# Optimization experiments

Hardware: AMD Instinct MI355X
Metric: run time of the kernel (lower is better)

Reference implementation:

```python
import jax, jax.numpy as jnp
import numpy as np

SIZE = 128      # reconstruction grid (size x size)
ANGLES = 128    # number of projection angles after interpolation
B, C, H, W = 2, 8, 128, 128  # batch, channels, detector rows (z-slices), detector cols
N_VIEWS = 8


def setup_inputs() -> dict:
    key = jax.random.key(0)
    keys = jax.random.split(key, N_VIEWS)
    return {f"f{i}": jax.random.normal(keys[i], (B, C, H, W), dtype=jnp.float32)
            for i in range(N_VIEWS)}


def _fbp(projections, size, n_angles):
    # projections: (B, C, H, V, W) -- V stacked views, W detector columns
    b, c, h, v, w = projections.shape
    # Interpolation step: resize V views -> n_angles angles (linear, half-pixel,
    # matching F.interpolate default semantics)
    sino = jax.image.resize(projections, (b, c, h, n_angles, w), method="linear")
    # Ram-Lak ramp filter along the detector-column axis
    ramp = jnp.abs(jnp.fft.fftfreq(w)).astype(jnp.float32)
    filt = jnp.real(jnp.fft.ifft(jnp.fft.fft(sino, axis=-1) * ramp, axis=-1)).astype(sino.dtype)
    # Back-projection (parallel beam, per z-slice H)
    thetas = jnp.arange(n_angles, dtype=jnp.float32) * (jnp.pi / n_angles)
    xs = jnp.arange(size, dtype=jnp.float32) - (size - 1) / 2.0
    X, Y = jnp.meshgrid(xs, xs, indexing="xy")  # (S, S)
    center = (w - 1) / 2.0

    sino_per_angle = jnp.moveaxis(filt, 3, 0)  # (A, B, C, H, W)

    def body(acc, inputs):
        theta, sino_a = inputs                       # sino_a: (B, C, H, W)
        t = X * jnp.cos(theta) + Y * jnp.sin(theta) + center  # (S, S)
        t = jnp.clip(t, 0.0, w - 1.0)
        t0 = jnp.floor(t).astype(jnp.int32)
        t1 = jnp.minimum(t0 + 1, w - 1)
        w1 = (t - t0).astype(sino_a.dtype)
        v0 = sino_a[..., t0]                         # (B, C, H, S, S) gather
        v1 = sino_a[..., t1]
        acc = acc + v0 * (1.0 - w1) + v1 * w1
        return acc, None

    acc0 = jnp.zeros((b, c, h, size, size), dtype=sino.dtype)
    vol, _ = jax.lax.scan(body, acc0, (thetas, sino_per_angle))
    return vol * (jnp.pi / (2.0 * n_angles))


def reference(f0, f1, f2, f3, f4, f5, f6, f7):
    # torch.cat([f.unsqueeze(3) for f in features], dim=3) == stack on new axis 3
    projections = jnp.stack([f0, f1, f2, f3, f4, f5, f6, f7], axis=3)  # (B,C,H,V,W)
    return _fbp(projections, SIZE, ANGLES)
```

## Files before the change

### kernel.cpp

```cpp
#include <hip/hip_runtime.h>
#include <math.h>

#define W 128
#define NANG 128
#define SZ 128
#define NV 8
#define NROWS 2048
#define K_DIM 1024
#define NPIX 16384
#define OUT_SCALE 0.012271846303085130f

typedef _Float16 f16x8 __attribute__((ext_vector_type(8)));
typedef _Float16 f16x4 __attribute__((ext_vector_type(4)));
typedef float    f32x4 __attribute__((ext_vector_type(4)));

#define PF_OFF 36864
#define WV_OFF (36864 + (size_t)NROWS * K_DIM * 2)

struct Ptrs8 { const float* p[8]; };

__device__ __forceinline__ void glds16(const void* g, void* l) {
    __builtin_amdgcn_global_load_lds(
        (const __attribute__((address_space(1))) void*)g,
        (__attribute__((address_space(3))) void*)l, 16, 0, 0);
}

#define FS_A 136
#define PREP_FG_BLOCKS 256

union PrepLds {
    struct {
        _Float16 sA[64 * FS_A];
        _Float16 sB[128 * FS_A];
        float    kl[W];
    } fg;
    struct {
        float  wrow[8 * K_DIM];
        float2 cst[NANG];
    } wv;
};

__global__ __launch_bounds__(256)
void k_prep(Ptrs8 in, _Float16* __restrict__ pf, _Float16* __restrict__ wv) {
    __shared__ PrepLds u;
    const int tid = threadIdx.x;

    if (blockIdx.x < PREP_FG_BLOCKS) {
        const int blk  = blockIdx.x;
        const int lane = tid & 63, wave = tid >> 6;
        const int fr = lane & 15, fg = lane >> 4;

        if (tid < W) {
            const int d = tid;
            const float w0 = 6.283185307179586f / (float)W * (float)d;
            float s = 0.f;
            for (int f = 1; f < 64; ++f)
                s = fmaf((float)f, __cosf(w0 * (float)f), s);
            s = 2.f * s + 64.f * ((d & 1) ? -1.f : 1.f);
            u.fg.kl[d] = s * (1.f / (float)(W * W));
        }
        {
            const int i   = tid >> 5;
            const int pos = (tid & 31) * 4;
#pragma unroll
            for (int v = 0; v < NV; ++v) {
                float4 x = *(const float4*)(in.p[v] + (size_t)(blk * 8 + i) * W + pos);
                f16x4 h = { (_Float16)x.x, (_Float16)x.y, (_Float16)x.z, (_Float16)x.w };
                *(f16x4*)&u.fg.sA[(i * 8 + v) * FS_A + pos] = h;
            }
        }
        __syncthreads();
        for (int e = tid; e < W * W; e += 256) {
            const int t = e >> 7, s = e & 127;
            u.fg.sB[t * FS_A + s] = (_Float16)u.fg.kl[(t - s) & (W - 1)];
        }
        __syncthreads();

        f32x4 acc[8] = {};
#pragma unroll
        for (int kb = 0; kb < W; kb += 32) {
            f16x8 af = *(const f16x8*)&u.fg.sA[(wave * 16 + fr) * FS_A + kb + fg * 8];
#pragma unroll
            for (int nt = 0; nt < 8; ++nt) {
                f16x8 bf = *(const f16x8*)&u.fg.sB[(nt * 16 + fr) * FS_A + kb + fg * 8];
                acc[nt] = __builtin_amdgcn_mfma_f32_16x16x32_f16(af, bf, acc[nt], 0, 0, 0);
            }
        }
#pragma unroll
        for (int nt = 0; nt < 8; ++nt) {
            int m = blk * 64 + wave * 16 + fg * 4;
            int n = nt * 16 + fr;
#pragma unroll
            for (int rr = 0; rr < 4; ++rr)
                pf[(size_t)(m + rr) * W + n] = (_Float16)acc[nt][rr];
        }
    } else {
        const int p0 = (blockIdx.x - PREP_FG_BLOCKS) * 8;
        if (tid < NANG) {
            float th = (float)tid * ((float)M_PI / (float)NANG);
            u.wv.cst[tid] = make_float2(cosf(th), sinf(th));
        }
        for (int i = tid; i < 8 * K_DIM; i += 256) u.wv.wrow[i] = 0.f;
        __syncthreads();
        const int px  = tid >> 5;
        const int sub = tid & 31;
        const int p = p0 + px;
        const float x = (float)(p & 127) - 63.5f;
        const float y = (float)(p >> 7) - 63.5f;
        float* prow = &u.wv.wrow[px * K_DIM];
        for (int a = sub; a < NANG; a += 32) {
            float2 c = u.wv.cst[a];
            float t = fmaf(x, c.x, fmaf(y, c.y, 63.5f));
            t = fminf(fmaxf(t, 0.f), 127.f);
            float tf = fminf(floorf(t), 126.f);
            int   ti = (int)tf;
            float wt = t - tf;
            float src = ((float)a + 0.5f) * 0.0625f - 0.5f;
            src = fminf(fmaxf(src, 0.f), 7.f);
            float vf = floorf(src);
            int   v0 = (int)vf;
            int   v1 = v0 + 1 < NV ? v0 + 1 : NV - 1;
            float wa = src - vf;
            float wA0 = (1.f - wa) * OUT_SCALE;
            atomicAdd(&prow[v0 * W + ti],     wA0 * (1.f - wt));
            atomicAdd(&prow[v0 * W + ti + 1], wA0 * wt);
            if (v1 != v0) {
                float wA1 = wa * OUT_SCALE;
                atomicAdd(&prow[v1 * W + ti],     wA1 * (1.f - wt));
                atomicAdd(&prow[v1 * W + ti + 1], wA1 * wt);
            }
        }
        __syncthreads();
        uint* wvu = (uint*)(wv + (size_t)p0 * K_DIM);
#pragma unroll
        for (int j = 0; j < 16; ++j) {
            int j2 = tid + 256 * j;
            float2 w2 = *(const float2*)&u.wv.wrow[j2 * 2];
            union { uint uu; struct { _Float16 lo, hi; } h; } pk;
            pk.h.lo = (_Float16)w2.x; pk.h.hi = (_Float16)w2.y;
            wvu[j2] = pk.uu;
        }
    }
}

#define NT3 32

__device__ __forceinline__ void fencebar() {
    asm volatile("" ::: "memory");
    __builtin_amdgcn_s_barrier();
    asm volatile("" ::: "memory");
}

__device__ __forceinline__ void stage3(const _Float16* __restrict__ G, int R0,
                                       int kt, _Float16* L, int tid) {
#pragma unroll
    for (int r = 0; r < 2; ++r) {
        const int c   = r * 256 + tid;
        const int row = c >> 2;
        const int q   = c & 3;
        const _Float16* src = G + (size_t)(R0 + row) * K_DIM + kt * 32
                                + ((q ^ ((row >> 1) & 3)) << 3);
        _Float16* dst = L + ((r * 256 + (tid & 192)) << 3);
        glds16(src, dst);
    }
}

__device__ __forceinline__ f16x8 frag3(const _Float16* L, int row, int q) {
    return *(const f16x8*)(L + row * 32 + ((q ^ ((row >> 1) & 3)) << 3));
}

__global__ __launch_bounds__(256, 4)
void k_gemm(const _Float16* __restrict__ A,
            const _Float16* __restrict__ Bm,
            float* __restrict__ out) {
    __shared__ _Float16 lds[16384];
    const int tid  = threadIdx.x;
    const int lane = tid & 63, wid = tid >> 6;
    const int wm = wid >> 1, wn = wid & 1;
    const int fr = lane & 15, fg = lane >> 4;

    const int flat = blockIdx.x;
    const int x    = flat & 7;
    const int idx  = flat >> 3;
    const int m0 = (idx & 15) * 128;
    const int n0 = (x * 16 + (idx >> 4)) * 128;

    _Float16* const A0 = lds;
    _Float16* const B0 = lds + 4096;
    _Float16* const A1 = lds + 8192;
    _Float16* const B1 = lds + 12288;

    stage3(A,  m0, 0, A0, tid);
    stage3(Bm, n0, 0, B0, tid);
    asm volatile("s_waitcnt vmcnt(0)" ::: "memory");
    fencebar();

    f32x4 acc[4][4] = {};
    f16x8 af[4], bf[4];
    const int ar = wm * 64 + fr;
    const int br = wn * 64 + fr;

    auto tile = [&](int t, _Float16* Ab, _Float16* Bb, _Float16* An, _Float16* Bn)
        __attribute__((always_inline)) {
        if (t + 1 < NT3) {
            stage3(A,  m0, t + 1, An, tid);
            stage3(Bm, n0, t + 1, Bn, tid);
        }
#pragma unroll
        for (int i = 0; i < 4; ++i) af[i] = frag3(Ab, ar + i * 16, fg);
#pragma unroll
        for (int j = 0; j < 4; ++j) bf[j] = frag3(Bb, br + j * 16, fg);
        __builtin_amdgcn_s_setprio(1);
#pragma unroll
        for (int i = 0; i < 4; ++i)
#pragma unroll
            for (int j = 0; j < 4; ++j)
                acc[i][j] = __builtin_amdgcn_mfma_f32_16x16x32_f16(
                    af[i], bf[j], acc[i][j], 0, 0, 0);
        __builtin_amdgcn_s_setprio(0);
        asm volatile("s_waitcnt lgkmcnt(0)" ::: "memory");
        if (t + 1 < NT3)
            asm volatile("s_waitcnt vmcnt(0)" ::: "memory");
        fencebar();
    };

    for (int tt = 0; tt < NT3; tt += 2) {
        tile(tt,     A0, B0, A1, B1);
        tile(tt + 1, A1, B1, A0, B0);
    }

#pragma unroll
    for (int i = 0; i < 4; ++i) {
#pragma unroll
        for (int j = 0; j < 4; ++j) {
            const int m = m0 + wm * 64 + i * 16 + fg * 4;
            const int n = n0 + wn * 64 + j * 16 + fr;
            float* op = out + (size_t)m * NPIX + n;
#pragma unroll
            for (int rr = 0; rr < 4; ++rr)
                op[(size_t)rr * NPIX] = acc[i][j][rr];
        }
    }
}

extern "C" void kernel_launch(void* const* d_in, const int* in_sizes, int n_in,
                              void* d_out, int out_size, void* d_ws, size_t ws_size,
                              hipStream_t stream) {
    _Float16*   pf = (_Float16*)((char*)d_ws + PF_OFF);
    _Float16*   wv = (_Float16*)((char*)d_ws + WV_OFF);

    Ptrs8 in;
    for (int i = 0; i < NV; ++i) in.p[i] = (const float*)d_in[i];

    k_prep<<<PREP_FG_BLOCKS + NPIX / 8, 256, 0, stream>>>(in, pf, wv);
    k_gemm<<<(NROWS / 128) * (NPIX / 128), 256, 0, stream>>>(pf, wv, (float*)d_out);
}
```

Baseline: 259.8 us.

## Switch GEMM to 32x32x16 MFMA and slim prep kernel LDS usage

The main GEMM moves from 16x16x32 MFMA tiles to 32x32x16 tiles. This halves the number of fragment loads per k-step and raises compute per LDS read. The prep kernel drops the circulant filter matrix from LDS and builds B fragments directly from the kernel vector. It also processes 4 pixels per weight block instead of 8 and computes cos/sin inline, which cuts LDS footprint and should raise occupancy. The trade-off is more redundant ALU work in prep and a different output store pattern in the GEMM epilogue.

```diff
diff --git a/kernel.cpp b/kernel.cpp
--- a/kernel.cpp
+++ b/kernel.cpp
@@ -13,6 +13,7 @@
 typedef _Float16 f16x8 __attribute__((ext_vector_type(8)));
 typedef _Float16 f16x4 __attribute__((ext_vector_type(4)));
 typedef float    f32x4 __attribute__((ext_vector_type(4)));
+typedef float    f32x16 __attribute__((ext_vector_type(16)));
 
 #define PF_OFF 36864
 #define WV_OFF (36864 + (size_t)NROWS * K_DIM * 2)
@@ -27,16 +28,15 @@
 
 #define FS_A 136
 #define PREP_FG_BLOCKS 256
+#define WVPIX 4
 
 union PrepLds {
     struct {
         _Float16 sA[64 * FS_A];
-        _Float16 sB[128 * FS_A];
         float    kl[W];
     } fg;
     struct {
-        float  wrow[8 * K_DIM];
-        float2 cst[NANG];
+        float wrow[WVPIX * K_DIM];
     } wv;
 };
 
@@ -70,19 +70,19 @@
             }
         }
         __syncthreads();
-        for (int e = tid; e < W * W; e += 256) {
-            const int t = e >> 7, s = e & 127;
-            u.fg.sB[t * FS_A + s] = (_Float16)u.fg.kl[(t - s) & (W - 1)];
-        }
-        __syncthreads();
 
         f32x4 acc[8] = {};
 #pragma unroll
         for (int kb = 0; kb < W; kb += 32) {
             f16x8 af = *(const f16x8*)&u.fg.sA[(wave * 16 + fr) * FS_A + kb + fg * 8];
+            const int sbase = kb + fg * 8;
 #pragma unroll
             for (int nt = 0; nt < 8; ++nt) {
-                f16x8 bf = *(const f16x8*)&u.fg.sB[(nt * 16 + fr) * FS_A + kb + fg * 8];
+                const int t_ = nt * 16 + fr;
+                f16x8 bf;
+#pragma unroll
+                for (int j = 0; j < 8; ++j)
+                    bf[j] = (_Float16)u.fg.kl[(t_ - sbase - j) & (W - 1)];
                 acc[nt] = __builtin_amdgcn_mfma_f32_16x16x32_f16(af, bf, acc[nt], 0, 0, 0);
             }
         }
@@ -95,22 +95,19 @@
                 pf[(size_t)(m + rr) * W + n] = (_Float16)acc[nt][rr];
         }
     } else {
-        const int p0 = (blockIdx.x - PREP_FG_BLOCKS) * 8;
-        if (tid < NANG) {
-            float th = (float)tid * ((float)M_PI / (float)NANG);
-            u.wv.cst[tid] = make_float2(cosf(th), sinf(th));
-        }
-        for (int i = tid; i < 8 * K_DIM; i += 256) u.wv.wrow[i] = 0.f;
+        const int p0 = (blockIdx.x - PREP_FG_BLOCKS) * WVPIX;
+        for (int i = tid; i < WVPIX * K_DIM; i += 256) u.wv.wrow[i] = 0.f;
         __syncthreads();
-        const int px  = tid >> 5;
-        const int sub = tid & 31;
+        const int px  = tid >> 6;
+        const int sub = tid & 63;
         const int p = p0 + px;
         const float x = (float)(p & 127) - 63.5f;
         const float y = (float)(p >> 7) - 63.5f;
         float* prow = &u.wv.wrow[px * K_DIM];
-        for (int a = sub; a < NANG; a += 32) {
-            float2 c = u.wv.cst[a];
-            float t = fmaf(x, c.x, fmaf(y, c.y, 63.5f));
+        for (int a = sub; a < NANG; a += 64) {
+            const float th = (float)a * ((float)M_PI / (float)NANG);
+            const float cx = cosf(th), cy = sinf(th);
+            float t = fmaf(x, cx, fmaf(y, cy, 63.5f));
             t = fminf(fmaxf(t, 0.f), 127.f);
             float tf = fminf(floorf(t), 126.f);
             int   ti = (int)tf;
@@ -133,7 +130,7 @@
         __syncthreads();
         uint* wvu = (uint*)(wv + (size_t)p0 * K_DIM);
 #pragma unroll
-        for (int j = 0; j < 16; ++j) {
+        for (int j = 0; j < 8; ++j) {
             int j2 = tid + 256 * j;
             float2 w2 = *(const float2*)&u.wv.wrow[j2 * 2];
             union { uint uu; struct { _Float16 lo, hi; } h; } pk;
@@ -177,7 +174,7 @@
     const int tid  = threadIdx.x;
     const int lane = tid & 63, wid = tid >> 6;
     const int wm = wid >> 1, wn = wid & 1;
-    const int fr = lane & 15, fg = lane >> 4;
+    const int l31 = lane & 31, hi = lane >> 5;
 
     const int flat = blockIdx.x;
     const int x    = flat & 7;
@@ -195,10 +192,10 @@
     asm volatile("s_waitcnt vmcnt(0)" ::: "memory");
     fencebar();
 
-    f32x4 acc[4][4] = {};
-    f16x8 af[4], bf[4];
-    const int ar = wm * 64 + fr;
-    const int br = wn * 64 + fr;
+    f32x16 acc[2][2] = {};
+    f16x8 af[2][2], bf[2][2];
+    const int ar = wm * 64 + l31;
+    const int br = wn * 64 + l31;
 
     auto tile = [&](int t, _Float16* Ab, _Float16* Bb, _Float16* An, _Float16* Bn)
         __attribute__((always_inline)) {
@@ -207,16 +204,25 @@
             stage3(Bm, n0, t + 1, Bn, tid);
         }
 #pragma unroll
-        for (int i = 0; i < 4; ++i) af[i] = frag3(Ab, ar + i * 16, fg);
-#pragma unroll
-        for (int j = 0; j < 4; ++j) bf[j] = frag3(Bb, br + j * 16, fg);
+        for (int i = 0; i < 2; ++i)
+#pragma unroll
+            for (int kc = 0; kc < 2; ++kc)
+                af[i][kc] = frag3(Ab, ar + i * 32, kc * 2 + hi);
+#pragma unroll
+        for (int j = 0; j < 2; ++j)
+#pragma unroll
+            for (int kc = 0; kc < 2; ++kc)
+                bf[j][kc] = frag3(Bb, br + j * 32, kc * 2 + hi);
         __builtin_amdgcn_s_setprio(1);
 #pragma unroll
-        for (int i = 0; i < 4; ++i)
-#pragma unroll
-            for (int j = 0; j < 4; ++j)
-                acc[i][j] = __builtin_amdgcn_mfma_f32_16x16x32_f16(
-                    af[i], bf[j], acc[i][j], 0, 0, 0);
+        for (int i = 0; i < 2; ++i)
+#pragma unroll
+            for (int j = 0; j < 2; ++j) {
+                acc[i][j] = __builtin_amdgcn_mfma_f32_32x32x16_f16(
+                    af[i][0], bf[j][0], acc[i][j], 0, 0, 0);
+                acc[i][j] = __builtin_amdgcn_mfma_f32_32x32x16_f16(
+                    af[i][1], bf[j][1], acc[i][j], 0, 0, 0);
+            }
         __builtin_amdgcn_s_setprio(0);
         asm volatile("s_waitcnt lgkmcnt(0)" ::: "memory");
         if (t + 1 < NT3)
@@ -230,15 +236,18 @@
     }
 
 #pragma unroll
-    for (int i = 0; i < 4; ++i) {
-#pragma unroll
-        for (int j = 0; j < 4; ++j) {
-            const int m = m0 + wm * 64 + i * 16 + fg * 4;
-            const int n = n0 + wn * 64 + j * 16 + fr;
-            float* op = out + (size_t)m * NPIX + n;
-#pragma unroll
-            for (int rr = 0; rr < 4; ++rr)
-                op[(size_t)rr * NPIX] = acc[i][j][rr];
+    for (int i = 0; i < 2; ++i) {
+#pragma unroll
+        for (int j = 0; j < 2; ++j) {
+            const int n = n0 + wn * 64 + j * 32 + l31;
+#pragma unroll
+            for (int rg = 0; rg < 4; ++rg) {
+#pragma unroll
+                for (int rr = 0; rr < 4; ++rr) {
+                    const int m = m0 + wm * 64 + i * 32 + rr + rg * 8 + 4 * hi;
+                    out[(size_t)m * NPIX + n] = acc[i][j][rg * 4 + rr];
+                }
+            }
         }
     }
 }
@@ -252,6 +261,6 @@
     Ptrs8 in;
     for (int i = 0; i < NV; ++i) in.p[i] = (const float*)d_in[i];
 
-    k_prep<<<PREP_FG_BLOCKS + NPIX / 8, 256, 0, stream>>>(in, pf, wv);
+    k_prep<<<PREP_FG_BLOCKS + NPIX / WVPIX, 256, 0, stream>>>(in, pf, wv);
     k_gemm<<<(NROWS / 128) * (NPIX / 128), 256, 0, stream>>>(pf, wv, (float*)d_out);
 }
```

Result: no change. 260.7 us (+0.3%).
